# Optimization experiments

Measured on AMD Instinct MI355X. Metric: run time of the kernel, lower is better.

## Reference

```python
import jax, jax.numpy as jnp
import numpy as np

DIM = 1024
HEADS = 16
HEAD_DIM = DIM // HEADS
SCALE = DIM ** (-0.5)  # NOTE: module scales by full dim, not head dim


def setup_inputs() -> dict:
    key = jax.random.key(0)
    k1, k2, k3, k4 = jax.random.split(key, 4)
    x = jax.random.normal(k1, (4, 2048, DIM), dtype=jnp.float32)
    w_qkv = jax.random.normal(k2, (DIM, 3 * DIM), dtype=jnp.float32) * (DIM ** -0.5)
    w_out = jax.random.normal(k3, (DIM, DIM), dtype=jnp.float32) * (DIM ** -0.5)
    b_out = jax.random.normal(k4, (DIM,), dtype=jnp.float32) * 0.01
    return {"x": x, "w_qkv": w_qkv, "w_out": w_out, "b_out": b_out}


def reference(x, w_qkv, w_out, b_out):
    b, n, _ = x.shape
    qkv = x @ w_qkv  # [b, n, 3*dim]
    # 'b n (qkv h d) -> qkv b h n d'
    qkv = qkv.reshape(b, n, 3, HEADS, HEAD_DIM).transpose(2, 0, 3, 1, 4)
    q, k, v = qkv[0], qkv[1], qkv[2]  # each [b, h, n, d]
    dots = jnp.einsum('bhid,bhjd->bhij', q, k) * SCALE
    attn = jax.nn.softmax(dots, axis=-1)
    out = jnp.einsum('bhij,bhjd->bhid', attn, v)
    out = out.transpose(0, 2, 1, 3).reshape(b, n, DIM)  # 'b h n d -> b n (h d)'
    return out @ w_out + b_out
```

## Files before the change

kernel.cpp:

```cpp
#include <hip/hip_runtime.h>
#include <math.h>

#define BATCH 4
#define SEQ   2048
#define DMODEL 1024
#define HEADS 16
#define DHEAD 64
#define SCALE 0.03125f
#define KEXP  0.045084220027780106f
#define QKV_ELEMS (BATCH * HEADS * SEQ * DHEAD)

typedef __attribute__((ext_vector_type(8))) short short8;
typedef __attribute__((ext_vector_type(4))) float floatx4;
typedef unsigned int u32;

__device__ __forceinline__ unsigned short f2bf(float f) {
  union { float f; unsigned u; } v;
  v.f = f;
  return (unsigned short)((v.u + 0x7FFFu + ((v.u >> 16) & 1u)) >> 16);
}

__device__ __forceinline__ float fast_exp2(float x) {
#if __has_builtin(__builtin_amdgcn_exp2f)
  return __builtin_amdgcn_exp2f(x);
#else
  return __expf(x * 0.6931471805599453f);
#endif
}

__device__ __forceinline__ u32 pack_bf16(float p0, float p1) {
#if __has_builtin(__builtin_amdgcn_cvt_pk_bf16_f32)
  typedef __bf16 bf16x2 __attribute__((ext_vector_type(2)));
  bf16x2 t = __builtin_amdgcn_cvt_pk_bf16_f32(p0, p1);
  u32 r;
  __builtin_memcpy(&r, &t, 4);
  return r;
#else
  u32 a0 = __float_as_uint(p0) + 0x8000u;
  u32 a1 = __float_as_uint(p1) + 0x8000u;
  return __builtin_amdgcn_perm(a1, a0, 0x07060302);
#endif
}

__device__ __forceinline__ void async_ld16(const void* g, void* l) {
  __builtin_amdgcn_global_load_lds(
      (const __attribute__((address_space(1))) u32*)g,
      (__attribute__((address_space(3))) u32*)l, 16, 0, 0);
}

__device__ __forceinline__ void trans_tile(const float* __restrict__ W,
                                           unsigned short* __restrict__ WT,
                                           int K, int N, int n0, int k0,
                                           float (*tile)[33]) {
  const int tx = threadIdx.x & 31, ty = threadIdx.x >> 5;
#pragma unroll
  for (int i = 0; i < 4; ++i)
    tile[ty + i * 8][tx] = W[(size_t)(k0 + ty + i * 8) * N + n0 + tx];
  __syncthreads();
#pragma unroll
  for (int i = 0; i < 4; ++i)
    WT[(size_t)(n0 + ty + i * 8) * K + k0 + tx] = f2bf(tile[tx][ty + i * 8]);
}

__global__ __launch_bounds__(256) void prep_kernel(
    const float* __restrict__ x, const float* __restrict__ wqkv,
    const float* __restrict__ wout, unsigned short* __restrict__ xb,
    unsigned short* __restrict__ wqkvT, unsigned short* __restrict__ woutT) {
  __shared__ float tile[32][33];
  const int bx = blockIdx.x;
  if (bx < 8192) {
    size_t i = ((size_t)bx * 256 + threadIdx.x) * 4;
    float4 v = *(const float4*)(x + i);
    ushort4 o;
    o.x = f2bf(v.x); o.y = f2bf(v.y); o.z = f2bf(v.z); o.w = f2bf(v.w);
    *(ushort4*)(xb + i) = o;
  } else if (bx < 11264) {
    int t = bx - 8192;
    trans_tile(wqkv, wqkvT, 1024, 3072, (t % 96) * 32, (t / 96) * 32, tile);
  } else {
    int t = bx - 11264;
    trans_tile(wout, woutT, 1024, 1024, (t % 32) * 32, (t / 32) * 32, tile);
  }
}

#define G_BAR() __builtin_amdgcn_s_barrier()
#define G_LGKM0() asm volatile("s_waitcnt lgkmcnt(0)" ::: "memory")

#define STAGE_TILE(t)                                                          \
  do {                                                                         \
    const unsigned short* Ab =                                                 \
        A + (size_t)(m0 + srow) * 1024 + (t) * 64 + schunk * 8;                \
    const unsigned short* Bb =                                                 \
        BT + (size_t)(n0 + srow) * 1024 + (t) * 64 + schunk * 8;               \
    unsigned short* sa = smemS + ((t) % 3) * 24576;                            \
    unsigned short* sb = sa + 16384;                                           \
    async_ld16(Ab, sa + tid * 8);                                              \
    async_ld16(Ab + 64 * 1024, sa + 4096 + tid * 8);                           \
    async_ld16(Ab + 128 * 1024, sa + 8192 + tid * 8);                          \
    async_ld16(Ab + 192 * 1024, sa + 12288 + tid * 8);                         \
    async_ld16(Bb, sb + tid * 8);                                              \
    async_ld16(Bb + 64 * 1024, sb + 4096 + tid * 8);                           \
  } while (0)

#define RD_A(SAp, mh)                                                          \
  do {                                                                         \
    _Pragma("unroll") for (int mi = 0; mi < 4; ++mi) {                         \
      a[mi][0] = *(const short8*)((SAp) + rowA + (mh)*4096 + mi * 1024 + cof0);\
      a[mi][1] = *(const short8*)((SAp) + rowA + (mh)*4096 + mi * 1024 + cof1);\
    }                                                                          \
  } while (0)

#define RD_B(SBp)                                                              \
  do {                                                                         \
    _Pragma("unroll") for (int ni = 0; ni < 2; ++ni) {                         \
      b[ni][0] = *(const short8*)((SBp) + rowB + ni * 1024 + cof0);            \
      b[ni][1] = *(const short8*)((SBp) + rowB + ni * 1024 + cof1);            \
    }                                                                          \
  } while (0)

#define CLUSTER(mh)                                                            \
  do {                                                                         \
    __builtin_amdgcn_s_setprio(1);                                             \
    _Pragma("unroll") for (int mi = 0; mi < 4; ++mi) {                         \
      _Pragma("unroll") for (int ni = 0; ni < 2; ++ni) {                       \
        acc[(mh)*4 + mi][ni] = __builtin_amdgcn_mfma_f32_16x16x32_bf16(        \
            a[mi][0], b[ni][0], acc[(mh)*4 + mi][ni], 0, 0, 0);                \
        acc[(mh)*4 + mi][ni] = __builtin_amdgcn_mfma_f32_16x16x32_bf16(        \
            a[mi][1], b[ni][1], acc[(mh)*4 + mi][ni], 0, 0, 0);                \
      }                                                                        \
    }                                                                          \
    __builtin_amdgcn_s_setprio(0);                                             \
  } while (0)

__device__ __forceinline__ void core256x128(
    const unsigned short* __restrict__ A, const unsigned short* __restrict__ BT,
    unsigned short* smemS, int m0, int n0, floatx4 (&acc)[8][2]) {
  const int tid = threadIdx.x;
  const int wave = tid >> 6, lane = tid & 63;
  const int Q4 = lane >> 4, L = lane & 15;
  const int wr = wave >> 2, wc = wave & 3;
  const int srow = tid >> 3;
  const int schunk = (tid & 7) ^ (srow & 7);
  const int xorL = L & 7;
  const int cof0 = (Q4 ^ xorL) * 8;
  const int cof1 = ((4 + Q4) ^ xorL) * 8;
  const int rowA = wr * 8192 + L * 64;
  const int rowB = wc * 2048 + L * 64;

  short8 a[4][2], b[2][2];
#pragma unroll
  for (int mt = 0; mt < 8; ++mt)
#pragma unroll
    for (int nt = 0; nt < 2; ++nt) acc[mt][nt] = (floatx4){0.f, 0.f, 0.f, 0.f};

  STAGE_TILE(0);
  STAGE_TILE(1);
  asm volatile("s_waitcnt vmcnt(6)" ::: "memory");
  G_BAR();

#pragma unroll
  for (int u = 0; u < 16; ++u) {
    unsigned short* SA = smemS + (u % 3) * 24576;
    unsigned short* SB = SA + 16384;
    RD_A(SA, 0);
    RD_B(SB);
    if (u + 2 < 16) STAGE_TILE(u + 2);
    G_BAR(); G_LGKM0();
    CLUSTER(0);
    G_BAR();
    RD_A(SA, 1);
    G_BAR(); G_LGKM0();
    CLUSTER(1);
    if (u + 2 < 16) asm volatile("s_waitcnt vmcnt(6)" ::: "memory");
    else            asm volatile("s_waitcnt vmcnt(0)" ::: "memory");
    G_BAR();
  }
}

#define K32_STAGE(t)                                                           \
  do {                                                                         \
    const unsigned short* Ab =                                                 \
        A + (size_t)(m0 + rA) * 1024 + (t) * 32 + cS;                          \
    const unsigned short* Bb =                                                 \
        BT + (size_t)(n0 + rA) * 1024 + (t) * 32 + cS;                         \
    unsigned short* sa = smemS + ((t) % 3) * 12288;                            \
    unsigned short* sb = sa + 8192;                                            \
    async_ld16(Ab, sa + tid * 8);                                              \
    async_ld16(Ab + 128 * 1024, sa + 4096 + tid * 8);                          \
    async_ld16(Bb, sb + tid * 8);                                              \
  } while (0)

__device__ __forceinline__ void core256x128_k32(
    const unsigned short* __restrict__ A, const unsigned short* __restrict__ BT,
    unsigned short* smemS, int m0, int n0, floatx4 (&acc)[8][2]) {
  const int tid = threadIdx.x;
  const int wave = tid >> 6, lane = tid & 63;
  const int Q4 = lane >> 4, L = lane & 15;
  const int wr = wave >> 2, wc = wave & 3;
  const int rA = tid >> 2;
  const int cS = ((tid & 3) ^ (rA & 3)) * 8;
  const int xq = (Q4 ^ (L & 3)) * 8;
  const int rowA = wr * 4096 + L * 32;
  const int rowB = wc * 1024 + L * 32;

  short8 a[8], b[2];
#pragma unroll
  for (int mt = 0; mt < 8; ++mt)
#pragma unroll
    for (int nt = 0; nt < 2; ++nt) acc[mt][nt] = (floatx4){0.f, 0.f, 0.f, 0.f};

  K32_STAGE(0);
  K32_STAGE(1);
  asm volatile("s_waitcnt vmcnt(3)" ::: "memory");
  G_BAR();

#pragma unroll
  for (int u = 0; u < 32; ++u) {
    unsigned short* SA = smemS + (u % 3) * 12288;
    unsigned short* SB = SA + 8192;
#pragma unroll
    for (int mt = 0; mt < 8; ++mt)
      a[mt] = *(const short8*)(SA + rowA + mt * 512 + xq);
#pragma unroll
    for (int nt = 0; nt < 2; ++nt)
      b[nt] = *(const short8*)(SB + rowB + nt * 512 + xq);
    if (u + 2 < 32) K32_STAGE(u + 2);
    G_BAR(); G_LGKM0();
    __builtin_amdgcn_s_setprio(1);
#pragma unroll
    for (int mt = 0; mt < 8; ++mt)
#pragma unroll
      for (int nt = 0; nt < 2; ++nt)
        acc[mt][nt] = __builtin_amdgcn_mfma_f32_16x16x32_bf16(
            a[mt], b[nt], acc[mt][nt], 0, 0, 0);
    __builtin_amdgcn_s_setprio(0);
    if (u + 2 < 32) asm volatile("s_waitcnt vmcnt(3)" ::: "memory");
    else            asm volatile("s_waitcnt vmcnt(0)" ::: "memory");
    G_BAR();
  }
}

__global__ __launch_bounds__(512, 4) void gemm_qkv_kernel(
    const unsigned short* __restrict__ A, const unsigned short* __restrict__ BT,
    unsigned short* __restrict__ qk, unsigned short* __restrict__ vtg) {
  __shared__ __align__(16) unsigned char smem[73728];
  unsigned short* smemS = (unsigned short*)smem;

  const int tid = threadIdx.x;
  const int wave = tid >> 6, lane = tid & 63;
  const int Q4 = lane >> 4, L = lane & 15;
  const int wr = wave >> 2, wc = wave & 3;

  const int flat = blockIdx.y * 24 + blockIdx.x;
  const int swz = (flat & 7) * 96 + (flat >> 3);
  const int mblk = swz / 24, nblk = swz % 24;
  const int m0 = mblk * 256, n0 = nblk * 128;

  floatx4 acc[8][2];
  core256x128_k32(A, BT, smemS, m0, n0, acc);

  const int bb = m0 >> 11;
  const int ntok0 = m0 & 2047;
  unsigned short* T = smemS;

  if (nblk < 16) {
    const float qsc = (nblk < 8) ? KEXP : 1.0f;
    unsigned short* dst = qk + (size_t)(nblk >> 3) * QKV_ELEMS;
    const int h0 = (nblk & 7) * 2;
#pragma unroll
    for (int mt = 0; mt < 8; ++mt)
#pragma unroll
      for (int nt = 0; nt < 2; ++nt) {
        const int col = wc * 32 + nt * 16 + L;
        const int tokl = wr * 128 + mt * 16 + Q4 * 4;
#pragma unroll
        for (int r = 0; r < 4; ++r)
          T[(tokl + r) * 136 + col] = f2bf(acc[mt][nt][r] * qsc);
      }
    __syncthreads();
#pragma unroll
    for (int it2 = 0; it2 < 8; ++it2) {
      int slot = it2 * 512 + tid;
      int tok = slot >> 4, ch = slot & 15;
      int hh = ch >> 3, inner = ch & 7;
      *(short8*)(dst +
                 (((size_t)((bb * 16 + h0 + hh) * 2048 + ntok0 + tok)) << 6) +
                 inner * 8) = *(const short8*)&T[tok * 136 + hh * 64 + inner * 8];
    }
  } else {
    const int nv0 = (nblk - 16) * 128;
#pragma unroll
    for (int mt = 0; mt < 8; ++mt)
#pragma unroll
      for (int nt = 0; nt < 2; ++nt) {
        const int col = wc * 32 + nt * 16 + L;
#pragma unroll
        for (int r = 0; r < 4; ++r) {
          int tok = wr * 128 + mt * 16 + Q4 * 4 + r;
          int pcm = (tok & ~31) | ((tok & 15) << 1) | ((tok >> 4) & 1);
          T[col * 264 + pcm] = f2bf(acc[mt][nt][r]);
        }
      }
    __syncthreads();
#pragma unroll
    for (int it2 = 0; it2 < 8; ++it2) {
      int slot = it2 * 512 + tid;
      int col = slot >> 5, ch = slot & 31;
      int nc = nv0 + col;
      *(short8*)(vtg +
                 (((size_t)((bb * 16 + (nc >> 6)) * 64 + (nc & 63))) << 11) +
                 ntok0 + ch * 8) = *(const short8*)&T[col * 264 + ch * 8];
    }
  }
}

__global__ __launch_bounds__(512, 2) void gemm_out_kernel(
    const unsigned short* __restrict__ A, const unsigned short* __restrict__ BT,
    const float* __restrict__ bias, float* __restrict__ C) {
  __shared__ __align__(16) unsigned char smem[147456];
  unsigned short* smemS = (unsigned short*)smem;

  const int tid = threadIdx.x;
  const int wave = tid >> 6, lane = tid & 63;
  const int Q4 = lane >> 4, L = lane & 15;
  const int wr = wave >> 2, wc = wave & 3;

  const int flat = blockIdx.y * 8 + blockIdx.x;
  const int swz = (flat & 7) * 32 + (flat >> 3);
  const int m0 = (swz >> 3) * 256, n0 = (swz & 7) * 128;

  floatx4 acc[8][2];
  core256x128(A, BT, smemS, m0, n0, acc);

#pragma unroll
  for (int mt = 0; mt < 8; ++mt) {
#pragma unroll
    for (int nt = 0; nt < 2; ++nt) {
      int nc = n0 + wc * 32 + nt * 16 + L;
      float bv = bias[nc];
#pragma unroll
      for (int r = 0; r < 4; ++r) {
        int m = m0 + wr * 128 + mt * 16 + Q4 * 4 + r;
        C[(size_t)m * DMODEL + nc] = acc[mt][nt][r] + bv;
      }
    }
  }
}

#undef STAGE_TILE
#undef RD_A
#undef RD_B
#undef CLUSTER
#undef K32_STAGE
#undef G_BAR
#undef G_LGKM0

__global__ __launch_bounds__(512, 4) void attn_kernel(
    const unsigned short* __restrict__ Qb, const unsigned short* __restrict__ Kb,
    const unsigned short* __restrict__ Vtg, unsigned short* __restrict__ Op) {
  __shared__ __align__(16) unsigned short Ks[2][64 * 64];
  __shared__ __align__(16) unsigned short Vs[2][64 * 64];
  const int tid = threadIdx.x;
  const int wave = tid >> 6, lane = tid & 63;
  const int quad = lane >> 4, l16 = lane & 15;
  const int bh = blockIdx.x & 63, qt = blockIdx.x >> 6;
  const size_t base = (size_t)bh * SEQ * DHEAD;
  const int lrow = lane >> 3, ls = lane & 7;
  const int dblk = ls ^ (lrow & 7);
  const int sw = l16 & 7;

  const unsigned short* kbase = Kb + base;
  const unsigned short* vbase = Vtg + base;
  const int rowS = wave * 8 + lrow;

  short8 onesf;
#pragma unroll
  for (int i = 0; i < 8; ++i) onesf[i] = (short)0x3F80;

  short8 qf[2][2];
#pragma unroll
  for (int qs = 0; qs < 2; ++qs) {
    int qrow = qt * 256 + wave * 32 + qs * 16 + l16;
    qf[qs][0] = *(const short8*)(Qb + base + (size_t)qrow * DHEAD + quad * 8);
    qf[qs][1] =
        *(const short8*)(Qb + base + (size_t)qrow * DHEAD + 32 + quad * 8);
  }

  floatx4 o[2][4], lacc[2];
#pragma unroll
  for (int qs = 0; qs < 2; ++qs) {
    lacc[qs] = (floatx4){0.f, 0.f, 0.f, 0.f};
#pragma unroll
    for (int dt = 0; dt < 4; ++dt) o[qs][dt] = (floatx4){0.f, 0.f, 0.f, 0.f};
  }

#define STAGE(buf, kc)                                                         \
  do {                                                                         \
    async_ld16(kbase + (size_t)((kc)*64 + rowS) * DHEAD + dblk * 8,            \
               &Ks[buf][wave * 512]);                                          \
    async_ld16(vbase + (size_t)rowS * SEQ + (kc)*64 + dblk * 8,                \
               &Vs[buf][wave * 512]);                                          \
  } while (0)

#define COMPUTE(buf)                                                           \
  do {                                                                         \
    _Pragma("unroll") for (int kc2 = 0; kc2 < 2; ++kc2) {                      \
      const int krow = kc2 * 32;                                               \
      short8 kf00 =                                                            \
          *(short8*)(&Ks[buf][0] + (krow + l16) * 64 + ((quad ^ sw) * 8));     \
      short8 kf01 = *(short8*)(&Ks[buf][0] + (krow + l16) * 64 +               \
                               (((4 + quad) ^ sw) * 8));                       \
      short8 kf10 = *(short8*)(&Ks[buf][0] + (krow + 16 + l16) * 64 +          \
                               ((quad ^ sw) * 8));                             \
      short8 kf11 = *(short8*)(&Ks[buf][0] + (krow + 16 + l16) * 64 +          \
                               (((4 + quad) ^ sw) * 8));                       \
      short8 vf[4];                                                            \
      _Pragma("unroll") for (int dt = 0; dt < 4; ++dt) vf[dt] =                \
          *(short8*)(&Vs[buf][0] + (dt * 16 + l16) * 64 +                      \
                     (((kc2 * 4 + quad) ^ sw) * 8));                           \
      floatx4 s0[2], s1[2];                                                    \
      _Pragma("unroll") for (int qs = 0; qs < 2; ++qs) {                       \
        s0[qs] = (floatx4){0.f, 0.f, 0.f, 0.f};                                \
        s1[qs] = (floatx4){0.f, 0.f, 0.f, 0.f};                                \
        s0[qs] = __builtin_amdgcn_mfma_f32_16x16x32_bf16(kf00, qf[qs][0],      \
                                                         s0[qs], 0, 0, 0);     \
        s0[qs] = __builtin_amdgcn_mfma_f32_16x16x32_bf16(kf01, qf[qs][1],      \
                                                         s0[qs], 0, 0, 0);     \
        s1[qs] = __builtin_amdgcn_mfma_f32_16x16x32_bf16(kf10, qf[qs][0],      \
                                                         s1[qs], 0, 0, 0);     \
        s1[qs] = __builtin_amdgcn_mfma_f32_16x16x32_bf16(kf11, qf[qs][1],      \
                                                         s1[qs], 0, 0, 0);     \
      }                                                                        \
      short8 pf[2];                                                            \
      _Pragma("unroll") for (int qs = 0; qs < 2; ++qs) {                       \
        union { short8 s8; u32 u[4]; } pu;                                     \
        _Pragma("unroll") for (int r = 0; r < 4; ++r) {                        \
          pu.u[r] = pack_bf16(fast_exp2(s0[qs][r]), fast_exp2(s1[qs][r]));     \
        }                                                                      \
        pf[qs] = pu.s8;                                                        \
      }                                                                        \
      _Pragma("unroll") for (int qs = 0; qs < 2; ++qs) {                       \
        lacc[qs] = __builtin_amdgcn_mfma_f32_16x16x32_bf16(pf[qs], onesf,      \
                                                           lacc[qs], 0, 0, 0); \
        _Pragma("unroll") for (int dt = 0; dt < 4; ++dt) o[qs][dt] =           \
            __builtin_amdgcn_mfma_f32_16x16x32_bf16(pf[qs], vf[dt],            \
                                                    o[qs][dt], 0, 0, 0);       \
      }                                                                        \
    }                                                                          \
  } while (0)

  STAGE(0, 0);
  for (int kc = 0; kc < SEQ / 64; kc += 2) {
    __syncthreads();
    if (kc + 1 < SEQ / 64) STAGE(1, kc + 1);
    COMPUTE(0);
    __syncthreads();
    if (kc + 2 < SEQ / 64) STAGE(0, kc + 2);
    COMPUTE(1);
  }
#undef STAGE
#undef COMPUTE

  const int b = bh >> 4, h = bh & 15;
#pragma unroll
  for (int qs = 0; qs < 2; ++qs) {
#pragma unroll
    for (int r = 0; r < 4; ++r) {
      float inv = 1.f / lacc[qs][r];
      int n = qt * 256 + wave * 32 + qs * 16 + quad * 4 + r;
      size_t rowbase = ((size_t)(b * SEQ + n)) * DMODEL + h * DHEAD;
#pragma unroll
      for (int dt = 0; dt < 4; ++dt)
        Op[rowbase + dt * 16 + l16] = f2bf(o[qs][dt][r] * inv);
    }
  }
}

extern "C" void kernel_launch(void* const* d_in, const int* in_sizes, int n_in,
                              void* d_out, int out_size, void* d_ws,
                              size_t ws_size, hipStream_t stream) {
  const float* x = (const float*)d_in[0];
  const float* w_qkv = (const float*)d_in[1];
  const float* w_out = (const float*)d_in[2];
  const float* b_out = (const float*)d_in[3];
  float* out = (float*)d_out;

  unsigned short* ws = (unsigned short*)d_ws;
  unsigned short* xb = ws;
  unsigned short* wqkvT = xb + 8388608;
  unsigned short* woutT = wqkvT + 3145728;
  unsigned short* qb = woutT + 1048576;
  unsigned short* kb = qb + QKV_ELEMS;
  unsigned short* vtg = kb + QKV_ELEMS;
  unsigned short* op = vtg + QKV_ELEMS;

  prep_kernel<<<dim3(12288), dim3(256), 0, stream>>>(x, w_qkv, w_out, xb,
                                                     wqkvT, woutT);
  gemm_qkv_kernel<<<dim3(24, 32), dim3(512), 0, stream>>>(xb, wqkvT, qb, vtg);
  attn_kernel<<<dim3(512), dim3(512), 0, stream>>>(qb, kb, vtg, op);
  gemm_out_kernel<<<dim3(8, 32), dim3(512), 0, stream>>>(op, woutT, b_out, out);
}
```

Before: 241.7 us.

## Retile output projection GEMM to 128x128 tiles with 256 threads and K32 staging

```diff
diff --git a/kernel.cpp b/kernel.cpp
--- a/kernel.cpp
+++ b/kernel.cpp
@@ -86,97 +86,6 @@
 #define G_BAR() __builtin_amdgcn_s_barrier()
 #define G_LGKM0() asm volatile("s_waitcnt lgkmcnt(0)" ::: "memory")
 
-#define STAGE_TILE(t)                                                          \
-  do {                                                                         \
-    const unsigned short* Ab =                                                 \
-        A + (size_t)(m0 + srow) * 1024 + (t) * 64 + schunk * 8;                \
-    const unsigned short* Bb =                                                 \
-        BT + (size_t)(n0 + srow) * 1024 + (t) * 64 + schunk * 8;               \
-    unsigned short* sa = smemS + ((t) % 3) * 24576;                            \
-    unsigned short* sb = sa + 16384;                                           \
-    async_ld16(Ab, sa + tid * 8);                                              \
-    async_ld16(Ab + 64 * 1024, sa + 4096 + tid * 8);                           \
-    async_ld16(Ab + 128 * 1024, sa + 8192 + tid * 8);                          \
-    async_ld16(Ab + 192 * 1024, sa + 12288 + tid * 8);                         \
-    async_ld16(Bb, sb + tid * 8);                                              \
-    async_ld16(Bb + 64 * 1024, sb + 4096 + tid * 8);                           \
-  } while (0)
-
-#define RD_A(SAp, mh)                                                          \
-  do {                                                                         \
-    _Pragma("unroll") for (int mi = 0; mi < 4; ++mi) {                         \
-      a[mi][0] = *(const short8*)((SAp) + rowA + (mh)*4096 + mi * 1024 + cof0);\
-      a[mi][1] = *(const short8*)((SAp) + rowA + (mh)*4096 + mi * 1024 + cof1);\
-    }                                                                          \
-  } while (0)
-
-#define RD_B(SBp)                                                              \
-  do {                                                                         \
-    _Pragma("unroll") for (int ni = 0; ni < 2; ++ni) {                         \
-      b[ni][0] = *(const short8*)((SBp) + rowB + ni * 1024 + cof0);            \
-      b[ni][1] = *(const short8*)((SBp) + rowB + ni * 1024 + cof1);            \
-    }                                                                          \
-  } while (0)
-
-#define CLUSTER(mh)                                                            \
-  do {                                                                         \
-    __builtin_amdgcn_s_setprio(1);                                             \
-    _Pragma("unroll") for (int mi = 0; mi < 4; ++mi) {                         \
-      _Pragma("unroll") for (int ni = 0; ni < 2; ++ni) {                       \
-        acc[(mh)*4 + mi][ni] = __builtin_amdgcn_mfma_f32_16x16x32_bf16(        \
-            a[mi][0], b[ni][0], acc[(mh)*4 + mi][ni], 0, 0, 0);                \
-        acc[(mh)*4 + mi][ni] = __builtin_amdgcn_mfma_f32_16x16x32_bf16(        \
-            a[mi][1], b[ni][1], acc[(mh)*4 + mi][ni], 0, 0, 0);                \
-      }                                                                        \
-    }                                                                          \
-    __builtin_amdgcn_s_setprio(0);                                             \
-  } while (0)
-
-__device__ __forceinline__ void core256x128(
-    const unsigned short* __restrict__ A, const unsigned short* __restrict__ BT,
-    unsigned short* smemS, int m0, int n0, floatx4 (&acc)[8][2]) {
-  const int tid = threadIdx.x;
-  const int wave = tid >> 6, lane = tid & 63;
-  const int Q4 = lane >> 4, L = lane & 15;
-  const int wr = wave >> 2, wc = wave & 3;
-  const int srow = tid >> 3;
-  const int schunk = (tid & 7) ^ (srow & 7);
-  const int xorL = L & 7;
-  const int cof0 = (Q4 ^ xorL) * 8;
-  const int cof1 = ((4 + Q4) ^ xorL) * 8;
-  const int rowA = wr * 8192 + L * 64;
-  const int rowB = wc * 2048 + L * 64;
-
-  short8 a[4][2], b[2][2];
-#pragma unroll
-  for (int mt = 0; mt < 8; ++mt)
-#pragma unroll
-    for (int nt = 0; nt < 2; ++nt) acc[mt][nt] = (floatx4){0.f, 0.f, 0.f, 0.f};
-
-  STAGE_TILE(0);
-  STAGE_TILE(1);
-  asm volatile("s_waitcnt vmcnt(6)" ::: "memory");
-  G_BAR();
-
-#pragma unroll
-  for (int u = 0; u < 16; ++u) {
-    unsigned short* SA = smemS + (u % 3) * 24576;
-    unsigned short* SB = SA + 16384;
-    RD_A(SA, 0);
-    RD_B(SB);
-    if (u + 2 < 16) STAGE_TILE(u + 2);
-    G_BAR(); G_LGKM0();
-    CLUSTER(0);
-    G_BAR();
-    RD_A(SA, 1);
-    G_BAR(); G_LGKM0();
-    CLUSTER(1);
-    if (u + 2 < 16) asm volatile("s_waitcnt vmcnt(6)" ::: "memory");
-    else            asm volatile("s_waitcnt vmcnt(0)" ::: "memory");
-    G_BAR();
-  }
-}
-
 #define K32_STAGE(t)                                                           \
   do {                                                                         \
     const unsigned short* Ab =                                                 \
@@ -314,44 +223,94 @@
   }
 }
 
-__global__ __launch_bounds__(512, 2) void gemm_out_kernel(
+#define K32O_STAGE(t)                                                          \
+  do {                                                                         \
+    const unsigned short* Ab =                                                 \
+        A + (size_t)(m0 + rA) * 1024 + (t) * 32 + cS;                          \
+    const unsigned short* Bb =                                                 \
+        BT + (size_t)(n0 + rA) * 1024 + (t) * 32 + cS;                         \
+    unsigned short* sa = smemS + ((t) % 3) * 8192;                             \
+    unsigned short* sb = sa + 4096;                                            \
+    async_ld16(Ab, sa + tid * 8);                                              \
+    async_ld16(Ab + 64 * 1024, sa + 2048 + tid * 8);                           \
+    async_ld16(Bb, sb + tid * 8);                                              \
+    async_ld16(Bb + 64 * 1024, sb + 2048 + tid * 8);                           \
+  } while (0)
+
+__global__ __launch_bounds__(256, 3) void gemm_out_kernel(
     const unsigned short* __restrict__ A, const unsigned short* __restrict__ BT,
     const float* __restrict__ bias, float* __restrict__ C) {
-  __shared__ __align__(16) unsigned char smem[147456];
+  __shared__ __align__(16) unsigned char smem[49152];
   unsigned short* smemS = (unsigned short*)smem;
 
   const int tid = threadIdx.x;
   const int wave = tid >> 6, lane = tid & 63;
   const int Q4 = lane >> 4, L = lane & 15;
-  const int wr = wave >> 2, wc = wave & 3;
+  const int wr = wave >> 1, wc = wave & 1;
+  const int rA = tid >> 2;
+  const int cS = ((tid & 3) ^ (rA & 3)) * 8;
+  const int xq = (Q4 ^ (L & 3)) * 8;
+  const int rowA = wr * 2048 + L * 32;
+  const int rowB = wc * 2048 + L * 32;
 
   const int flat = blockIdx.y * 8 + blockIdx.x;
-  const int swz = (flat & 7) * 32 + (flat >> 3);
-  const int m0 = (swz >> 3) * 256, n0 = (swz & 7) * 128;
-
-  floatx4 acc[8][2];
-  core256x128(A, BT, smemS, m0, n0, acc);
-
-#pragma unroll
-  for (int mt = 0; mt < 8; ++mt) {
-#pragma unroll
-    for (int nt = 0; nt < 2; ++nt) {
-      int nc = n0 + wc * 32 + nt * 16 + L;
+  const int swz = (flat & 7) * 64 + (flat >> 3);
+  const int m0 = (swz >> 3) * 128, n0 = (swz & 7) * 128;
+
+  short8 a[4], b[4];
+  floatx4 acc[4][4];
+#pragma unroll
+  for (int mt = 0; mt < 4; ++mt)
+#pragma unroll
+    for (int nt = 0; nt < 4; ++nt) acc[mt][nt] = (floatx4){0.f, 0.f, 0.f, 0.f};
+
+  K32O_STAGE(0);
+  K32O_STAGE(1);
+  asm volatile("s_waitcnt vmcnt(4)" ::: "memory");
+  G_BAR();
+
+#pragma unroll
+  for (int u = 0; u < 32; ++u) {
+    unsigned short* SA = smemS + (u % 3) * 8192;
+    unsigned short* SB = SA + 4096;
+#pragma unroll
+    for (int mt = 0; mt < 4; ++mt)
+      a[mt] = *(const short8*)(SA + rowA + mt * 512 + xq);
+#pragma unroll
+    for (int nt = 0; nt < 4; ++nt)
+      b[nt] = *(const short8*)(SB + rowB + nt * 512 + xq);
+    if (u + 2 < 32) K32O_STAGE(u + 2);
+    G_BAR(); G_LGKM0();
+    __builtin_amdgcn_s_setprio(1);
+#pragma unroll
+    for (int mt = 0; mt < 4; ++mt)
+#pragma unroll
+      for (int nt = 0; nt < 4; ++nt)
+        acc[mt][nt] = __builtin_amdgcn_mfma_f32_16x16x32_bf16(
+            a[mt], b[nt], acc[mt][nt], 0, 0, 0);
+    __builtin_amdgcn_s_setprio(0);
+    if (u + 2 < 32) asm volatile("s_waitcnt vmcnt(4)" ::: "memory");
+    else            asm volatile("s_waitcnt vmcnt(0)" ::: "memory");
+    G_BAR();
+  }
+
+#pragma unroll
+  for (int mt = 0; mt < 4; ++mt) {
+#pragma unroll
+    for (int nt = 0; nt < 4; ++nt) {
+      int nc = n0 + wc * 64 + nt * 16 + L;
       float bv = bias[nc];
 #pragma unroll
       for (int r = 0; r < 4; ++r) {
-        int m = m0 + wr * 128 + mt * 16 + Q4 * 4 + r;
+        int m = m0 + wr * 64 + mt * 16 + Q4 * 4 + r;
         C[(size_t)m * DMODEL + nc] = acc[mt][nt][r] + bv;
       }
     }
   }
 }
 
-#undef STAGE_TILE
-#undef RD_A
-#undef RD_B
-#undef CLUSTER
 #undef K32_STAGE
+#undef K32O_STAGE
 #undef G_BAR
 #undef G_LGKM0
 
@@ -498,5 +457,5 @@
                                                      wqkvT, woutT);
   gemm_qkv_kernel<<<dim3(24, 32), dim3(512), 0, stream>>>(xb, wqkvT, qb, vtg);
   attn_kernel<<<dim3(512), dim3(512), 0, stream>>>(qb, kb, vtg, op);
-  gemm_out_kernel<<<dim3(8, 32), dim3(512), 0, stream>>>(op, woutT, b_out, out);
-}
+  gemm_out_kernel<<<dim3(8, 64), dim3(256), 0, stream>>>(op, woutT, b_out, out);
+}
```

After: 242.7 us. Within noise of the previous version (+0.4%).
